# Kernel optimization log

Hardware: AMD Instinct MI355X
Metric: run time of the kernel (lower is better)

## Reference

```python
import jax, jax.numpy as jnp
import numpy as np

E, H, D = 1024, 16, 64
F = 4608          # max_ffn_size = int(1024*3*1.5)
BASE_FFN = 3072   # int(emb*3)
ADAPT = 0.5
CHUNK = 256


def rotate_half(x):
    x1 = x[..., ::2]
    x2 = x[..., 1::2]
    return jnp.stack((-x2, x1), axis=-1).reshape(x.shape[:-1] + (-1,))


def rms_norm(x, w, eps=1e-6):
    x = jnp.where(jnp.isnan(x) | jnp.isinf(x), jnp.zeros_like(x), x)
    rms = jnp.clip(jnp.sqrt(jnp.mean(x * x, axis=-1, keepdims=True) + eps), 1e-6, 1e6)
    return x / rms * w


def setup_inputs() -> dict:
    key = jax.random.key(0)
    ks = jax.random.split(key, 12)
    s = 0.02
    return {
        "x": jax.random.normal(ks[0], (2, 4096, E), dtype=jnp.float32),
        "w_qkv": jax.random.normal(ks[1], (E, 3 * E), dtype=jnp.float32) * s,
        "w_out": jax.random.normal(ks[2], (E, E), dtype=jnp.float32) * s,
        "g1": jnp.ones((E,), dtype=jnp.float32),
        "g2": jnp.ones((E,), dtype=jnp.float32),
        "w_dp1": jax.random.normal(ks[3], (E, E // 4), dtype=jnp.float32) * s,
        "w_dp2": jax.random.normal(ks[4], (E // 4, 1), dtype=jnp.float32) * s,
        "w_gate": jax.random.normal(ks[5], (E, F), dtype=jnp.float32) * s,
        "w_up": jax.random.normal(ks[6], (E, F), dtype=jnp.float32) * s,
        "w_down": jax.random.normal(ks[7], (F, E), dtype=jnp.float32) * s,
        "g_hidden": jnp.ones((F,), dtype=jnp.float32),
    }


def _linear_attention(x, w_qkv, w_out):
    B, L, _ = x.shape
    qkv = (x @ w_qkv).reshape(B, L, 3, H, D).transpose(2, 0, 3, 1, 4)  # [3,B,H,L,D]
    q, k, v = qkv[0], qkv[1], qkv[2]
    # RoPE (start_pos = 0)
    pos = jnp.arange(L, dtype=jnp.float32)
    inv_freq = 1.0 / (10000.0 ** (jnp.arange(0, D, 2, dtype=jnp.float32) / D))
    freqs = pos[:, None] * inv_freq[None, :]
    emb = jnp.concatenate([freqs, freqs], axis=-1)
    cos = jnp.cos(emb)[None, None]
    sin = jnp.sin(emb)[None, None]
    q = q * cos + rotate_half(q) * sin
    k = k * cos + rotate_half(k) * sin
    # elu + 1 feature map
    q = jax.nn.elu(q) + 1.0
    k = jax.nn.elu(k) + 1.0
    # chunk-wise cumulative recurrence (no cache path)
    NC = L // CHUNK
    def to_chunks(t):
        return jnp.moveaxis(t.reshape(B, H, NC, CHUNK, D), 2, 0)  # [NC,B,H,C,D]
    qc, kc, vc = to_chunks(q), to_chunks(k), to_chunks(v)

    def step(carry, inp):
        S, Z = carry  # S:[B,H,D,D], Z:[B,H,D]
        qi, ki, vi = inp
        kv = jnp.einsum('bhld,bhle->bhlde', ki, vi)
        kv_cum = jnp.cumsum(kv, axis=2) + S[:, :, None]
        k_cum = jnp.cumsum(ki, axis=2) + Z[:, :, None]
        num = jnp.einsum('bhld,bhlde->bhle', qi, kv_cum)
        den = jnp.einsum('bhld,bhld->bhl', qi, k_cum)
        return (kv_cum[:, :, -1], k_cum[:, :, -1]), (num, den)

    S0 = jnp.zeros((B, H, D, D), dtype=x.dtype)
    Z0 = jnp.zeros((B, H, D), dtype=x.dtype)
    _, (num, den) = jax.lax.scan(step, (S0, Z0), (qc, kc, vc))
    num = jnp.moveaxis(num, 0, 2).reshape(B, H, L, D)
    den = jnp.moveaxis(den, 0, 2).reshape(B, H, L)
    den = jnp.maximum(den, 1e-6)
    out = num / den[..., None]
    out = out.transpose(0, 2, 1, 3).reshape(B, L, H * D)
    return out @ w_out


def _adaptive_ffn(x, w_dp1, w_dp2, w_gate, w_up, w_down, g_hidden):
    x_mean = x.mean(axis=1)                                   # [B,E]
    dim_ratio = jax.nn.sigmoid(jax.nn.silu(x_mean @ w_dp1) @ w_dp2)  # [B,1]
    ratio = jnp.clip(1.0 + (dim_ratio - 0.5) * 2.0 * ADAPT, 1.0 - ADAPT, 1.0 + ADAPT)
    size = jnp.maximum(1, jnp.floor(BASE_FFN * ratio.mean())).astype(jnp.int32)
    mask = (jnp.arange(F) < size).astype(x.dtype)             # [F]
    gate = jax.nn.silu(x @ w_gate) * mask
    up = (x @ w_up) * mask
    hidden = gate * up
    hidden = jnp.where(jnp.isnan(hidden) | jnp.isinf(hidden), jnp.zeros_like(hidden), hidden)
    # RMSNorm over the first `size` features only (matches sliced torch RMSNorm)
    rms = jnp.sqrt(jnp.sum(hidden * hidden, axis=-1, keepdims=True) / size.astype(x.dtype) + 1e-6)
    rms = jnp.clip(rms, 1e-6, 1e6)
    hidden = hidden / rms * g_hidden * mask                   # padded-to-F hidden
    return hidden @ w_down


def reference(x, w_qkv, w_out, g1, g2, w_dp1, w_dp2, w_gate, w_up, w_down, g_hidden):
    # pre-norm residual block: x + attn(norm1(x)); then x + ffn(norm2(x))
    h = rms_norm(x, g1)
    x = x + _linear_attention(h, w_qkv, w_out)
    h2 = rms_norm(x, g2)
    x = x + _adaptive_ffn(h2, w_dp1, w_dp2, w_gate, w_up, w_down, g_hidden)
    return x
```

## Files before the change

kernel.cpp:

```cpp
#include <hip/hip_runtime.h>
#include <hip/hip_bf16.h>

#define Ee 1024
#define Hh 16
#define Ff 4608
#define Ll 4096
#define Bb 2
#define NCc 16
#define CHk 256

typedef short bf16x8 __attribute__((ext_vector_type(8)));
typedef float f32x4 __attribute__((ext_vector_type(4)));

#define GLD16(g, l) __builtin_amdgcn_global_load_lds( \
    (const __attribute__((address_space(1))) unsigned int*)(g), \
    (__attribute__((address_space(3))) unsigned int*)(l), 16, 0, 0)
#define SCHED0() __builtin_amdgcn_sched_barrier(0)
#define SBAR()   __builtin_amdgcn_s_barrier()

__device__ __forceinline__ unsigned short f2bf(float f){
  unsigned int u = __builtin_bit_cast(unsigned int, f);
  u += 0x7fffu + ((u >> 16) & 1u);
  return (unsigned short)(u >> 16);
}
__device__ __forceinline__ float bf2f(unsigned short h){
  unsigned int u = ((unsigned int)h) << 16;
  return __builtin_bit_cast(float, u);
}
__device__ __forceinline__ float fixv(float v){
  return (__builtin_isnan(v) || __builtin_isinf(v)) ? 0.f : v;
}

__global__ __launch_bounds__(256) void wconv_kernel(const float* __restrict__ W,
    unsigned short* __restrict__ WT, int K, int N, const float* __restrict__ scale){
  __shared__ unsigned short T[64][72];
  int k0 = blockIdx.y*64, n0 = blockIdx.x*64;
  int t = threadIdx.x;
  int kr = t>>4, n4 = (t&15)*4;
  #pragma unroll
  for (int it=0; it<4; it++){
    int k = kr + it*16;
    float s = scale ? scale[k0+k] : 1.f;
    float4 v = *(const float4*)(W + (size_t)(k0+k)*N + n0 + n4);
    T[n4+0][k] = f2bf(v.x*s);
    T[n4+1][k] = f2bf(v.y*s);
    T[n4+2][k] = f2bf(v.z*s);
    T[n4+3][k] = f2bf(v.w*s);
  }
  __syncthreads();
  int u = t&7;
  #pragma unroll
  for (int it=0; it<2; it++){
    int n = (t>>3) + it*32;
    *(bf16x8*)(WT + (size_t)(n0+n)*K + k0 + u*8) = *(const bf16x8*)&T[n][u*8];
  }
}

__global__ __launch_bounds__(256) void rmsnorm_kernel(const float* __restrict__ x,
    const float* __restrict__ g, unsigned short* __restrict__ out){
  int row = blockIdx.x; int t = threadIdx.x;
  float4 v = ((const float4*)(x + (size_t)row*Ee))[t];
  v.x=fixv(v.x); v.y=fixv(v.y); v.z=fixv(v.z); v.w=fixv(v.w);
  float ss = v.x*v.x + v.y*v.y + v.z*v.z + v.w*v.w;
  #pragma unroll
  for (int off=32; off>0; off>>=1) ss += __shfl_down(ss, off);
  __shared__ float red[4];
  if ((t&63)==0) red[t>>6] = ss;
  __syncthreads();
  float tot = red[0]+red[1]+red[2]+red[3];
  float rms = sqrtf(tot*(1.f/Ee) + 1e-6f);
  rms = fminf(fmaxf(rms, 1e-6f), 1e6f);
  float inv = 1.f/rms;
  float4 gv = ((const float4*)g)[t];
  uint2 o;
  o.x = (unsigned)f2bf(v.x*inv*gv.x) | ((unsigned)f2bf(v.y*inv*gv.y)<<16);
  o.y = (unsigned)f2bf(v.z*inv*gv.z) | ((unsigned)f2bf(v.w*inv*gv.w)<<16);
  ((uint2*)(out + (size_t)row*Ee))[t] = o;
}

template<int MODE>
__global__ __launch_bounds__(512) void gemm_kernel(
    const unsigned short* __restrict__ A, const unsigned short* __restrict__ Bt,
    void* __restrict__ Cv, int M, int N, int K,
    const float* __restrict__ res, const float* __restrict__ rowscale,
    const float* __restrict__ klim){
  __shared__ __align__(16) unsigned short S[36864];
  int tid = threadIdx.x;
  int nbx = gridDim.x;
  int id = blockIdx.y * nbx + blockIdx.x;
  int chunk = (nbx * gridDim.y) >> 3;
  int wg = (id & 7) * chunk + (id >> 3);
  int m0 = (wg / nbx) * 256, n0 = (wg % nbx) * 128;
  int lane = tid & 63, wave = tid >> 6;
  int wm = (wave>>1)*64, wn = (wave&1)*64;
  int lrow = lane & 15;
  int lksw = (((lane>>4) ^ ((lrow>>1)&3)))*8;
  float klim0 = (MODE==2 && klim) ? klim[0] : 0.f;
  int kend = K;
  if (MODE==2 && klim){
    int sz = (int)klim0;
    int ke = ((sz + 31) >> 5) << 5;
    kend = ke < K ? ke : K;
  }
  int nk = kend >> 5;
  int segr = lane >> 2;
  int cg = (((lane&3) ^ ((lane>>3)&3))) * 8;
  const unsigned short* gp[3];
  int loff[3];
  #pragma unroll
  for (int i=0;i<3;i++){
// ... 2 lines not shown
    else       { gp[i] = Bt + (size_t)(n0 + (g-16)*16 + segr)*K + cg;  loff[i] = 8192 + (g-16)*512; }
  }
  f32x4 acc[4][4] = {};
  #pragma unroll
  for (int i=0;i<3;i++) GLD16(gp[i], &S[loff[i]]);
  if (nk > 1){
    #pragma unroll
    for (int i=0;i<3;i++) GLD16(gp[i]+32, &S[12288 + loff[i]]);
  }
  SCHED0();
  if (nk > 1) asm volatile("s_waitcnt vmcnt(3)" ::: "memory");
  else        asm volatile("s_waitcnt vmcnt(0)" ::: "memory");
  SBAR(); SCHED0();
  int cur = 0;
  for (int t=0; t<nk; ++t){
    if (t+2 < nk){
      int stg = cur+2; if (stg>=3) stg-=3;
      int ko = (t+2) << 5;
      #pragma unroll
      for (int i=0;i<3;i++) GLD16(gp[i]+ko, &S[stg*12288 + loff[i]]);
    }
    int base = cur*12288;
    bf16x8 af[4], bfr[4];
    #pragma unroll
    for (int i=0;i<4;i++){
      af[i]  = *(const bf16x8*)&S[base + (wm + i*16 + lrow)*32 + lksw];
      bfr[i] = *(const bf16x8*)&S[base + 8192 + (wn + i*16 + lrow)*32 + lksw];
    }
    __builtin_amdgcn_s_setprio(1);
    #pragma unroll
    for (int mi=0;mi<4;mi++)
      #pragma unroll
      for (int ni=0;ni<4;ni++)
        acc[mi][ni] = __builtin_amdgcn_mfma_f32_16x16x32_bf16(af[mi], bfr[ni], acc[mi][ni], 0,0,0);
    __builtin_amdgcn_s_setprio(0);
    if (t+1 < nk){
      SCHED0();
      if (t+2 < nk) asm volatile("s_waitcnt vmcnt(3)" ::: "memory");
      else          asm volatile("s_waitcnt vmcnt(0)" ::: "memory");
      SBAR(); SCHED0();
    }
    cur = (cur==2) ? 0 : cur+1;
  }
  int lg = lane >> 4;
  int rbase = m0 + wm + (lg<<2);
  int cbase = n0 + wn + lrow;
  #pragma unroll
  for (int mi=0;mi<4;mi++){
    #pragma unroll
    for (int r=0;r<4;r++){
      int row = rbase + mi*16 + r;
      float rs = 1.f;
      if (MODE==2){
        float rms = sqrtf(rowscale[row]/klim0 + 1e-6f);
        rms = fminf(fmaxf(rms, 1e-6f), 1e6f);
        rs = 1.f/rms;
      }
      #pragma unroll
      for (int ni=0;ni<4;ni++){
        int col = cbase + ni*16;
        float v = acc[mi][ni][r];
        if (MODE==0){
          ((unsigned short*)Cv)[(size_t)row*N + col] = f2bf(v);
        } else if (MODE==1){
          ((float*)Cv)[(size_t)row*N + col] = v + res[(size_t)row*N + col];
        } else {
          ((float*)Cv)[(size_t)row*N + col] = v*rs + res[(size_t)row*N + col];
        }
      }
    }
  }
}

__global__ __launch_bounds__(512) void gateup_kernel(
    const unsigned short* __restrict__ A, const unsigned short* __restrict__ Gt,
    const unsigned short* __restrict__ Ut, unsigned short* __restrict__ Hid,
    const float* __restrict__ scal, float* __restrict__ sumsq){
  __shared__ __align__(16) unsigned short S[49152];
  int tid = threadIdx.x;
  int nbx = gridDim.x;
  int id = blockIdx.y * nbx + blockIdx.x;
  int chunk = (nbx * gridDim.y) >> 3;
  int wg = (id & 7) * chunk + (id >> 3);
  int m0 = (wg / nbx) * 256, n0 = (wg % nbx) * 128;
  int size = (int)scal[0];
  if (n0 >= size){
    int r = tid >> 1, cb = n0 + (tid&1)*64;
    unsigned short* hp = Hid + (size_t)(m0+r)*Ff + cb;
    bf16x8 z = {};
    #pragma unroll
    for (int i=0;i<8;i++) *(bf16x8*)(hp + i*8) = z;
    return;
  }
  int lane = tid & 63, wave = tid >> 6;
  int wm = (wave>>1)*64, wn = (wave&1)*64;
  int lrow = lane & 15;
  int lksw = (((lane>>4) ^ ((lrow>>1)&3)))*8;
  int segr = lane >> 2;
  int cg = (((lane&3) ^ ((lane>>3)&3))) * 8;
  const unsigned short* gp[4];
  int loff[4];
  #pragma unroll
  for (int i=0;i<4;i++){
    int g = wave*4 + i;
    if (g < 16)      { gp[i] = A  + (size_t)(m0 + g*16 + segr)*Ee + cg;       loff[i] = g*512; }
    else if (g < 24) { gp[i] = Gt + (size_t)(n0 + (g-16)*16 + segr)*Ee + cg;  loff[i] = 8192 + (g-16)*512; }
    else             { gp[i] = Ut + (size_t)(n0 + (g-24)*16 + segr)*Ee + cg;  loff[i] = 12288 + (g-24)*512; }
  }
  f32x4 ag[4][4] = {}, au[4][4] = {};
  #pragma unroll
  for (int i=0;i<4;i++) GLD16(gp[i], &S[loff[i]]);
  #pragma unroll
  for (int i=0;i<4;i++) GLD16(gp[i]+32, &S[16384 + loff[i]]);
  SCHED0();
  asm volatile("s_waitcnt vmcnt(4)" ::: "memory");
  SBAR(); SCHED0();
  int cur = 0;
  for (int t=0; t<32; ++t){
    if (t+2 < 32){
      int stg = cur+2; if (stg>=3) stg-=3;
      int ko = (t+2) << 5;
      #pragma unroll
      for (int i=0;i<4;i++) GLD16(gp[i]+ko, &S[stg*16384 + loff[i]]);
    }
    int base = cur*16384;
    bf16x8 af[4], bg4[4], bu4[4];
    #pragma unroll
    for (int i=0;i<4;i++){
      af[i]  = *(const bf16x8*)&S[base + (wm + i*16 + lrow)*32 + lksw];
      bg4[i] = *(const bf16x8*)&S[base + 8192  + (wn + i*16 + lrow)*32 + lksw];
      bu4[i] = *(const bf16x8*)&S[base + 12288 + (wn + i*16 + lrow)*32 + lksw];
    }
    __builtin_amdgcn_s_setprio(1);
    #pragma unroll
    for (int mi=0;mi<4;mi++)
      #pragma unroll
      for (int ni=0;ni<4;ni++){
        ag[mi][ni] = __builtin_amdgcn_mfma_f32_16x16x32_bf16(af[mi], bg4[ni], ag[mi][ni], 0,0,0);
        au[mi][ni] = __builtin_amdgcn_mfma_f32_16x16x32_bf16(af[mi], bu4[ni], au[mi][ni], 0,0,0);
      }
    __builtin_amdgcn_s_setprio(0);
    if (t+1 < 32){
      SCHED0();
      if (t+2 < 32) asm volatile("s_waitcnt vmcnt(4)" ::: "memory");
      else          asm volatile("s_waitcnt vmcnt(0)" ::: "memory");
      SBAR(); SCHED0();
    }
    cur = (cur==2) ? 0 : cur+1;
  }
  int lg = lane >> 4;
  int lr = lrow;
  int rbase = m0 + wm + (lg<<2);
  int cbase = n0 + wn + lr;
  #pragma unroll
  for (int mi=0;mi<4;mi++){
    #pragma unroll
    for (int r=0;r<4;r++){
      int row = rbase + mi*16 + r;
      float s4 = 0.f;
      #pragma unroll
      for (int ni=0;ni<4;ni++){
        int col = cbase + ni*16;
        float g = ag[mi][ni][r], u = au[mi][ni][r];
        float hv = (g * (1.f/(1.f+expf(-g)))) * u;
        if (col >= size) hv = 0.f;
        if (__builtin_isnan(hv) || __builtin_isinf(hv)) hv = 0.f;
        Hid[(size_t)row*Ff + col] = f2bf(hv);
        s4 += hv*hv;
      }
      s4 += __shfl_xor(s4, 1);
      s4 += __shfl_xor(s4, 2);
      s4 += __shfl_xor(s4, 4);
      s4 += __shfl_xor(s4, 8);
      if (lr == 0) atomicAdd(&sumsq[row], s4);
    }
  }
}

__global__ __launch_bounds__(256) void rope_kernel(unsigned short* __restrict__ qkv){
  size_t idx = (size_t)blockIdx.x*256 + threadIdx.x;
  int i = (int)(idx & 31);
  int h = (int)((idx>>5) & 15);
  size_t bl = idx >> 9;
  int pos = (int)(bl & (Ll-1));
  int d0 = 2*i, d1 = d0+1;
  size_t base = bl*3072 + (size_t)h*64 + d0;
  const float LOG1E4_D32 = 0.2878231366242557f;
  float e0 = (float)(d0 < 32 ? d0 : d0-32);
  float e1 = (float)(d1 < 32 ? d1 : d1-32);
  float f0 = pos * expf(-e0*LOG1E4_D32);
  float f1 = pos * expf(-e1*LOG1E4_D32);
  float s0,c0,s1,c1;
  sincosf(f0,&s0,&c0); sincosf(f1,&s1,&c1);
  unsigned int* qp = (unsigned int*)(qkv + base);
  unsigned int qv = *qp;
  float q0 = bf2f((unsigned short)(qv&0xffff)), q1 = bf2f((unsigned short)(qv>>16));
  float r0 = q0*c0 - q1*s0;
  float r1 = q1*c1 + q0*s1;
  r0 = r0>0.f ? r0+1.f : expf(r0);
  r1 = r1>0.f ? r1+1.f : expf(r1);
  *qp = (unsigned)f2bf(r0) | ((unsigned)f2bf(r1)<<16);
  unsigned int* kp = (unsigned int*)(qkv + base + 1024);
  unsigned int kv = *kp;
  float k0v = bf2f((unsigned short)(kv&0xffff)), k1v = bf2f((unsigned short)(kv>>16));
  float t0 = k0v*c0 - k1v*s0;
  float t1 = k1v*c1 + k0v*s1;
  t0 = t0>0.f ? t0+1.f : expf(t0);
  t1 = t1>0.f ? t1+1.f : expf(t1);
  *kp = (unsigned)f2bf(t0) | ((unsigned)f2bf(t1)<<16);
}

__global__ __launch_bounds__(256) void chunksum_kernel(const unsigned short* __restrict__ qkv,
    float* __restrict__ Ssum){
  __shared__ __align__(16) unsigned short Kt[64][72];
  __shared__ __align__(16) unsigned short Vt[80][72];
  int c = blockIdx.x, bh = blockIdx.y;
  int b = bh >> 4, h = bh & 15;
  int tid = threadIdx.x, lane = tid & 63, wave = tid >> 6;
  int lr = lane & 15, lg = lane >> 4;
  f32x4 acc[5] = {};
  {
    int r16 = tid >> 4, m4 = (tid & 15) * 4;
    unsigned short val = (r16 == 0) ? (unsigned short)0x3F80 : (unsigned short)0;
    #pragma unroll
    for (int u=0; u<4; u++) Vt[64 + r16][m4 + u] = val;
  }
  for (int t=0; t<4; ++t){
    __syncthreads();
    #pragma unroll
    for (int i=0; i<2; i++){
      int tau = tid + i*256;
      int m = tau & 63, dg = (tau >> 6) * 8;
      size_t g = ((size_t)(b*Ll + c*CHk + t*64 + m))*3072 + h*64 + dg;
      bf16x8 kv = *(const bf16x8*)(qkv + g + 1024);
      bf16x8 vv = *(const bf16x8*)(qkv + g + 2048);
      #pragma unroll
      for (int u=0; u<8; u++){
        Kt[dg+u][m] = (unsigned short)kv[u];
        Vt[dg+u][m] = (unsigned short)vv[u];
      }
    }
    __syncthreads();
    #pragma unroll
    for (int kk=0; kk<2; kk++){
      bf16x8 af = *(const bf16x8*)&Kt[wave*16 + lr][kk*32 + lg*8];
      #pragma unroll
      for (int ni=0; ni<5; ni++){
        bf16x8 vf = *(const bf16x8*)&Vt[ni*16 + lr][kk*32 + lg*8];
        acc[ni] = __builtin_amdgcn_mfma_f32_16x16x32_bf16(af, vf, acc[ni], 0,0,0);
      }
    }
  }
  float* S = Ssum + ((size_t)bh*NCc + c)*4160;
  int j = wave*16 + lg*4;
  #pragma unroll
  for (int ni=0; ni<4; ni++)
    #pragma unroll
    for (int r=0; r<4; r++)
      S[(size_t)(j+r)*64 + ni*16 + lr] = acc[ni][r];
  if (lr == 0){
    #pragma unroll
    for (int r=0; r<4; r++) S[4096 + j + r] = acc[4][r];
  }
}

__global__ __launch_bounds__(256) void prefix_kernel(const float* __restrict__ Ssum,
    float* __restrict__ Spre){
  int bh = blockIdx.x; int t = threadIdx.x;
  size_t base = (size_t)bh*NCc*4160;
  for (int e=t; e<4160; e+=256){
    float acc = 0.f;
    #pragma unroll
    for (int c=0;c<NCc;c++){
      Spre[base + (size_t)c*4160 + e] = acc;
      acc += Ssum[base + (size_t)c*4160 + e];
    }
  }
}

__global__ __launch_bounds__(256, 2) void attnout_kernel(const unsigned short* __restrict__ qkv,
    const float* __restrict__ Spre, unsigned short* __restrict__ attn){
  __shared__ __align__(16) unsigned short SpT[64][72];
// ... 13 lines not shown
    #pragma unroll
    for (int g8=0; g8<8; g8++){
      bf16x8 qv = *(const bf16x8*)(qp + g8*8);
      #pragma unroll
      for (int u=0; u<8; u++) zacc += bf2f((unsigned short)qv[u]) * Sp[4096 + g8*8 + u];
    }
    qZd[tid] = zacc;
  }
  #pragma unroll
  for (int i=0; i<2; i++){
    int tau = tid + i*256;
    int j = tau & 63, dg = (tau >> 6) * 8;
    const float* sp = Sp + j*64 + dg;
    #pragma unroll
    for (int u=0; u<8; u++) SpT[dg+u][j] = f2bf(sp[u]);
  }
  bf16x8 af[4][2];
  #pragma unroll
  for (int mi=0; mi<4; mi++){
    size_t qrow = ((size_t)(b*Ll + c*CHk + wave*64 + mi*16 + lr))*3072 + (size_t)h*64;
    #pragma unroll
    for (int kk=0; kk<2; kk++)
      af[mi][kk] = *(const bf16x8*)(qkv + qrow + kk*32 + lg*8);
  }
  __syncthreads();
  f32x4 accO[4][4] = {};
  #pragma unroll
  for (int kk=0; kk<2; kk++){
    #pragma unroll
    for (int ni=0; ni<4; ni++){
      bf16x8 bsp = *(const bf16x8*)&SpT[ni*16 + lr][kk*32 + lg*8];
      #pragma unroll
      for (int mi=0; mi<4; mi++)
        accO[mi][ni] = __builtin_amdgcn_mfma_f32_16x16x32_bf16(af[mi][kk], bsp, accO[mi][ni], 0,0,0);
    }
  }
  f32x4 den4[4] = {};
  for (int t=0; t<4; ++t){
    __syncthreads();
    #pragma unroll
    for (int i=0; i<2; i++){
      int tau = tid + i*256;
      int m = tau & 63, dg = (tau >> 6) * 8;
      size_t g = ((size_t)(b*Ll + c*CHk + t*64 + m))*3072 + h*64 + dg;
      *(bf16x8*)&Ks[m][dg] = *(const bf16x8*)(qkv + g + 1024);
      bf16x8 vv = *(const bf16x8*)(qkv + g + 2048);
      #pragma unroll
      for (int u=0; u<8; u++) Vt[dg+u][m] = (unsigned short)vv[u];
    }
    __syncthreads();
    if (wave < t) continue;
    f32x4 sacc[4][4] = {};
    #pragma unroll
    for (int kk=0; kk<2; kk++){
      #pragma unroll
      for (int ni=0; ni<4; ni++){
        bf16x8 kf = *(const bf16x8*)&Ks[ni*16 + lr][kk*32 + lg*8];
        #pragma unroll
        for (int mi=0; mi<4; mi++)
          sacc[mi][ni] = __builtin_amdgcn_mfma_f32_16x16x32_bf16(af[mi][kk], kf, sacc[mi][ni], 0,0,0);
      }
    }
    unsigned short (*Pw)[72] = P[wave];
    bool diag = (t == wave);
    #pragma unroll
    for (int mi=0; mi<4; mi++){
      #pragma unroll
      for (int r=0; r<4; r++){
        int q_l = mi*16 + lg*4 + r;
        float rs = 0.f;
        #pragma unroll
        for (int ni=0; ni<4; ni++){
          int m_l = ni*16 + lr;
          float v = sacc[mi][ni][r];
          if (diag && m_l > q_l) v = 0.f;
          rs += v;
          Pw[q_l][m_l] = f2bf(v);
        }
        rs += __shfl_xor(rs, 1);
        rs += __shfl_xor(rs, 2);
        rs += __shfl_xor(rs, 4);
        rs += __shfl_xor(rs, 8);
        den4[mi][r] += rs;
      }
    }
    #pragma unroll
    for (int kk=0; kk<2; kk++){
      bf16x8 pa[4], vf[4];
      #pragma unroll
      for (int mi=0; mi<4; mi++) pa[mi] = *(const bf16x8*)&Pw[mi*16 + lr][kk*32 + lg*8];
      #pragma unroll
      for (int ni=0; ni<4; ni++) vf[ni] = *(const bf16x8*)&Vt[ni*16 + lr][kk*32 + lg*8];
      #pragma unroll
      for (int mi=0; mi<4; mi++)
        #pragma unroll
        for (int ni=0; ni<4; ni++)
          accO[mi][ni] = __builtin_amdgcn_mfma_f32_16x16x32_bf16(pa[mi], vf[ni], accO[mi][ni], 0,0,0);
    }
  }
  #pragma unroll
  for (int mi=0; mi<4; mi++){
    #pragma unroll
    for (int r=0; r<4; r++){
      int q_l = mi*16 + lg*4 + r;
      float dtot = den4[mi][r] + qZd[wave*64 + q_l];
      float inv = 1.f / fmaxf(dtot, 1e-6f);
      size_t l = (size_t)(b*Ll + c*CHk + wave*64 + q_l);
      unsigned short* op = attn + l*Ee + h*64 + lr;
      #pragma unroll
      for (int ni=0; ni<4; ni++)
        op[ni*16] = f2bf(accO[mi][ni][r] * inv);
    }
  }
}

__global__ __launch_bounds__(256) void colmean1_kernel(const unsigned short* __restrict__ h2,
    float* __restrict__ partial){
  int e = blockIdx.x*256 + threadIdx.x;
  int ly = blockIdx.y;
  int b = blockIdx.z;
  int l0 = ly * 128;
  float s = 0.f;
  for (int l=l0; l<l0+128; l++) s += bf2f(h2[((size_t)(b*Ll + l))*Ee + e]);
  partial[((size_t)(b*32 + ly))*Ee + e] = s;
}
__global__ __launch_bounds__(256) void colmean2_kernel(const float* __restrict__ partial,
    float* __restrict__ xmean){
  int e = blockIdx.x*256 + threadIdx.x;
  int b = blockIdx.y;
  float s = 0.f;
// ... 28 lines not shown
  }
  if (t==0){
    float rm = 0.5f*(ratio_s[0]+ratio_s[1]);
    float size_f = floorf(3072.f * rm);
    if (size_f < 1.f) size_f = 1.f;
    scalars[0] = size_f;
  }
}

extern "C" void kernel_launch(void* const* d_in, const int* in_sizes, int n_in,
                              void* d_out, int out_size, void* d_ws, size_t ws_size,
                              hipStream_t stream){
  const float* x      = (const float*)d_in[0];
  const float* w_qkv  = (const float*)d_in[1];
  const float* w_out  = (const float*)d_in[2];
  const float* g1     = (const float*)d_in[3];
  const float* g2     = (const float*)d_in[4];
  const float* w_dp1  = (const float*)d_in[5];
  const float* w_dp2  = (const float*)d_in[6];
  const float* w_gate = (const float*)d_in[7];
  const float* w_up   = (const float*)d_in[8];
  const float* w_down = (const float*)d_in[9];
  const float* g_hid  = (const float*)d_in[10];
  float* out = (float*)d_out;

  char* w = (char*)d_ws;
  size_t o = 0;
  auto alloc = [&](size_t bytes)->char*{ char* p = w + o; o += (bytes + 255) & ~255ull; return p; };
  unsigned short* R1   = (unsigned short*)alloc((size_t)8192*1024*2);
  float*          x2   = (float*)alloc((size_t)8192*1024*4);
  char*           R2   = alloc((size_t)8192*4608*2);
  unsigned short* qkvT = (unsigned short*)alloc((size_t)3072*1024*2);
  unsigned short* outT = (unsigned short*)alloc((size_t)1024*1024*2);
  char*           W2   = alloc((size_t)3*4608*1024*2);
  float*       partial = (float*)alloc((size_t)64*1024*4);
  float*         xmean = (float*)alloc(2048*4);
  float*          scal = (float*)alloc(64);
  float*         sumsq = (float*)alloc(8192*4);

  unsigned short* qkv    = (unsigned short*)R2;
  unsigned short* hidden = (unsigned short*)R2;
  float* Ssum = (float*)W2;
  float* Spre = Ssum + (size_t)512*4160;
  unsigned short* gateT = (unsigned short*)W2;
  unsigned short* upT   = gateT + (size_t)4608*1024;
  unsigned short* downT = upT   + (size_t)4608*1024;

  wconv_kernel<<<dim3(3072/64, 1024/64),256,0,stream>>>(w_qkv, qkvT, 1024, 3072, nullptr);
  wconv_kernel<<<dim3(1024/64, 1024/64),256,0,stream>>>(w_out, outT, 1024, 1024, nullptr);

  rmsnorm_kernel<<<8192,256,0,stream>>>(x, g1, R1);
  gemm_kernel<0><<<dim3(3072/128, 8192/256),512,0,stream>>>(R1, qkvT, qkv,
      8192,3072,1024, nullptr,nullptr,nullptr);
  rope_kernel<<<16384,256,0,stream>>>(qkv);
  chunksum_kernel<<<dim3(NCc,Bb*Hh),256,0,stream>>>(qkv, Ssum);
  prefix_kernel<<<Bb*Hh,256,0,stream>>>(Ssum, Spre);
  attnout_kernel<<<dim3(NCc,Bb*Hh),256,0,stream>>>(qkv, Spre, R1);

  wconv_kernel<<<dim3(4608/64, 1024/64),256,0,stream>>>(w_gate, gateT, 1024, 4608, nullptr);
  wconv_kernel<<<dim3(4608/64, 1024/64),256,0,stream>>>(w_up,   upT,   1024, 4608, nullptr);
  wconv_kernel<<<dim3(1024/64, 4608/64),256,0,stream>>>(w_down, downT, 4608, 1024, g_hid);

  gemm_kernel<1><<<dim3(1024/128, 8192/256),512,0,stream>>>(R1, outT, x2,
      8192,1024,1024, x,nullptr,nullptr);
  rmsnorm_kernel<<<8192,256,0,stream>>>(x2, g2, R1);
  colmean1_kernel<<<dim3(4,32,2),256,0,stream>>>(R1, partial);
  colmean2_kernel<<<dim3(4,2),256,0,stream>>>(partial, xmean);
  dimpred_kernel<<<1,256,0,stream>>>(xmean, w_dp1, w_dp2, scal);
  hipMemsetAsync(sumsq, 0, 8192*sizeof(float), stream);
  gateup_kernel<<<dim3(4608/128, 8192/256),512,0,stream>>>(R1, gateT, upT, hidden, scal, sumsq);
  gemm_kernel<2><<<dim3(1024/128, 8192/256),512,0,stream>>>(hidden, downT, out,
      8192,1024,4608, x2, sumsq, scal);
}
```

Measured before the change: 482.6 us.

## Use 256x256 tiled 4-stage GEMM for QKV and interleaved gate/up projection

Adds a new 256x256-tile GEMM with a 4-stage LDS pipeline that splits each k-step into two half-MFMA phases with interleaved global-to-LDS loads, and uses it for the QKV projection. Gate and up weights are interleaved into one transposed matrix in 128-column blocks so the gate/up kernel runs as a single wide GEMM, then pairs the gate and up halves through LDS in the epilogue for SiLU, masking and the sum of squares. The larger tiles aim to raise arithmetic intensity and cut operand refetches. In exchange they add register and LDS pressure and an extra LDS-exchange epilogue with many barriers.

Result: slower. 635.0 us (+31.6%).

```diff
diff --git a/kernel.cpp b/kernel.cpp
--- a/kernel.cpp
+++ b/kernel.cpp
@@ -17,6 +17,7 @@
     (__attribute__((address_space(3))) unsigned int*)(l), 16, 0, 0)
 #define SCHED0() __builtin_amdgcn_sched_barrier(0)
 #define SBAR()   __builtin_amdgcn_s_barrier()
+#define MFMA16(a,b,c) __builtin_amdgcn_mfma_f32_16x16x32_bf16(a,b,c,0,0,0)
 
 __device__ __forceinline__ unsigned short f2bf(float f){
   unsigned int u = __builtin_bit_cast(unsigned int, f);
@@ -32,7 +33,7 @@
 }
 
 __global__ __launch_bounds__(256) void wconv_kernel(const float* __restrict__ W,
-    unsigned short* __restrict__ WT, int K, int N, const float* __restrict__ scale){
+    unsigned short* __restrict__ WT, int K, int N, const float* __restrict__ scale, int gu){
   __shared__ unsigned short T[64][72];
   int k0 = blockIdx.y*64, n0 = blockIdx.x*64;
   int t = threadIdx.x;
@@ -52,7 +53,10 @@
   #pragma unroll
   for (int it=0; it<2; it++){
     int n = (t>>3) + it*32;
-    *(bf16x8*)(WT + (size_t)(n0+n)*K + k0 + u*8) = *(const bf16x8*)&T[n][u*8];
+    int nn = n0 + n;
+    int nout = nn;
+    if (gu) nout = ((nn>>7)<<8) + (nn&127) + ((gu==2)?128:0);
+    *(bf16x8*)(WT + (size_t)nout*K + k0 + u*8) = *(const bf16x8*)&T[n][u*8];
   }
 }
 
@@ -76,6 +80,225 @@
   o.x = (unsigned)f2bf(v.x*inv*gv.x) | ((unsigned)f2bf(v.y*inv*gv.y)<<16);
   o.y = (unsigned)f2bf(v.z*inv*gv.z) | ((unsigned)f2bf(v.w*inv*gv.w)<<16);
   ((uint2*)(out + (size_t)row*Ee))[t] = o;
+}
+
+
+__global__ __launch_bounds__(512) void gemm8p_kernel(
+    const unsigned short* __restrict__ A, const unsigned short* __restrict__ Bt,
+    unsigned short* __restrict__ C, int M, int N, int K){
+  __shared__ __align__(16) unsigned short S[65536];
+  int tid = threadIdx.x;
+  int nbx = gridDim.x;
+  int id = blockIdx.y*nbx + blockIdx.x;
+  int chunk = (nbx*gridDim.y) >> 3;
+  int wg = (id&7)*chunk + (id>>3);
+  int m0 = (wg/nbx)*256, n0 = (wg%nbx)*256;
+  int lane = tid&63, wave = tid>>6;
+  int wm = (wave>>2)*128, wn = (wave&3)*64;
+  int lrow = lane&15, lg = lane>>4;
+  int lksw = (lg ^ ((lrow>>1)&3))*8;
+  int nk = K>>5;
+  int srow = tid>>2;
+  int scg = ((tid&3) ^ ((tid>>3)&3))*8;
+  const unsigned short* aA0 = A  + (size_t)(m0 + srow)*K + scg;
+  const unsigned short* aA1 = A  + (size_t)(m0 + 128 + srow)*K + scg;
+  const unsigned short* aB0 = Bt + (size_t)(n0 + srow)*K + scg;
+  const unsigned short* aB1 = Bt + (size_t)(n0 + 128 + srow)*K + scg;
+  int dA0 = wave*512, dA1 = 4096 + wave*512;
+  int dB0 = 8192 + wave*512, dB1 = 12288 + wave*512;
+  f32x4 acc[8][4] = {};
+  #pragma unroll
+  for (int p=0;p<3;p++){
+    int ko = p<<5; int bb = p*16384;
+    GLD16(aA0+ko, &S[bb+dA0]); GLD16(aA1+ko, &S[bb+dA1]);
+    GLD16(aB0+ko, &S[bb+dB0]); GLD16(aB1+ko, &S[bb+dB1]);
+  }
+  SCHED0();
+  asm volatile("s_waitcnt vmcnt(8)" ::: "memory");
+  SBAR(); SCHED0();
+  int cur = 0;
+  for (int t=0; t<nk; ++t){
+    int sb = ((cur+3)&3)*16384;
+    int ko = (t+3)<<5;
+    bool stg = (t+3 < nk);
+    int rb = cur*16384;
+    bf16x8 bf[4], af[4];
+    #pragma unroll
+    for (int j=0;j<4;j++) bf[j] = *(const bf16x8*)&S[rb + 8192 + (wn + j*16 + lrow)*32 + lksw];
+    #pragma unroll
+    for (int i=0;i<4;i++) af[i] = *(const bf16x8*)&S[rb + (wm + i*16 + lrow)*32 + lksw];
+    if (stg){ GLD16(aA0+ko, &S[sb+dA0]); GLD16(aA1+ko, &S[sb+dA1]); }
+    SCHED0(); SBAR();
+    asm volatile("s_waitcnt lgkmcnt(0)" ::: "memory");
+    SCHED0();
+    __builtin_amdgcn_s_setprio(1);
+    #pragma unroll
+    for (int i=0;i<4;i++)
+      #pragma unroll
+      for (int j=0;j<4;j++)
+        acc[i][j] = MFMA16(af[i], bf[j], acc[i][j]);
+    __builtin_amdgcn_s_setprio(0);
+    SCHED0(); SBAR();
+    #pragma unroll
+    for (int i=0;i<4;i++) af[i] = *(const bf16x8*)&S[rb + (wm + 64 + i*16 + lrow)*32 + lksw];
+    if (stg){ GLD16(aB0+ko, &S[sb+dB0]); GLD16(aB1+ko, &S[sb+dB1]); }
+    SCHED0();
+    if (t+3 < nk)      asm volatile("s_waitcnt vmcnt(8)" ::: "memory");
+    else if (t+2 < nk) asm volatile("s_waitcnt vmcnt(4)" ::: "memory");
+    else               asm volatile("s_waitcnt vmcnt(0)" ::: "memory");
+    SBAR();
+    asm volatile("s_waitcnt lgkmcnt(0)" ::: "memory");
+    SCHED0();
+    __builtin_amdgcn_s_setprio(1);
+    #pragma unroll
+    for (int i=0;i<4;i++)
+      #pragma unroll
+      for (int j=0;j<4;j++)
+        acc[4+i][j] = MFMA16(af[i], bf[j], acc[4+i][j]);
+    __builtin_amdgcn_s_setprio(0);
+    SCHED0(); SBAR();
+    cur = (cur+1)&3;
+  }
+  #pragma unroll
+  for (int mi=0;mi<8;mi++){
+    #pragma unroll
+    for (int r=0;r<4;r++){
+      int row = m0 + wm + mi*16 + lg*4 + r;
+      #pragma unroll
+      for (int ni=0;ni<4;ni++){
+        int col = n0 + wn + ni*16 + lrow;
+        C[(size_t)row*N + col] = f2bf(acc[mi][ni][r]);
+      }
+    }
+  }
+}
+
+__global__ __launch_bounds__(512) void gateup8p_kernel(
+    const unsigned short* __restrict__ A, const unsigned short* __restrict__ GUt,
+    unsigned short* __restrict__ Hid, const float* __restrict__ scal,
+    float* __restrict__ sumsq){
+  __shared__ __align__(16) unsigned short S[65536];
+  int tid = threadIdx.x;
+  int nbx = gridDim.x;
+  int id = blockIdx.y*nbx + blockIdx.x;
+  int chunk = (nbx*gridDim.y) >> 3;
+  int wg = (id&7)*chunk + (id>>3);
+  int m0 = (wg/nbx)*256, n0 = (wg%nbx)*256;
+  int n0r = (n0>>8)*128;
+  int size = (int)scal[0];
+  if (n0r >= size){
+    int r = tid >> 1, cb = n0r + (tid&1)*64;
+    unsigned short* hp = Hid + (size_t)(m0+r)*Ff + cb;
+    bf16x8 z = {};
+    #pragma unroll
+    for (int i=0;i<8;i++) *(bf16x8*)(hp + i*8) = z;
+    return;
+  }
+  int lane = tid&63, wave = tid>>6;
+  int wm = (wave>>2)*128, wn = (wave&3)*64;
+  int lrow = lane&15, lg = lane>>4;
+  int lksw = (lg ^ ((lrow>>1)&3))*8;
+  const int K = Ee, nk = Ee>>5;
+  int srow = tid>>2;
+  int scg = ((tid&3) ^ ((tid>>3)&3))*8;
+  const unsigned short* aA0 = A   + (size_t)(m0 + srow)*K + scg;
+  const unsigned short* aA1 = A   + (size_t)(m0 + 128 + srow)*K + scg;
+  const unsigned short* aB0 = GUt + (size_t)(n0 + srow)*K + scg;
+  const unsigned short* aB1 = GUt + (size_t)(n0 + 128 + srow)*K + scg;
+  int dA0 = wave*512, dA1 = 4096 + wave*512;
+  int dB0 = 8192 + wave*512, dB1 = 12288 + wave*512;
+  f32x4 acc[8][4] = {};
+  #pragma unroll
+  for (int p=0;p<3;p++){
+    int ko = p<<5; int bb = p*16384;
+    GLD16(aA0+ko, &S[bb+dA0]); GLD16(aA1+ko, &S[bb+dA1]);
+    GLD16(aB0+ko, &S[bb+dB0]); GLD16(aB1+ko, &S[bb+dB1]);
+  }
+  SCHED0();
+  asm volatile("s_waitcnt vmcnt(8)" ::: "memory");
+  SBAR(); SCHED0();
+  int cur = 0;
+  for (int t=0; t<nk; ++t){
+    int sb = ((cur+3)&3)*16384;
+    int ko = (t+3)<<5;
+    bool stg = (t+3 < nk);
+    int rb = cur*16384;
+    bf16x8 bf[4], af[4];
+    #pragma unroll
+    for (int j=0;j<4;j++) bf[j] = *(const bf16x8*)&S[rb + 8192 + (wn + j*16 + lrow)*32 + lksw];
+    #pragma unroll
+    for (int i=0;i<4;i++) af[i] = *(const bf16x8*)&S[rb + (wm + i*16 + lrow)*32 + lksw];
+    if (stg){ GLD16(aA0+ko, &S[sb+dA0]); GLD16(aA1+ko, &S[sb+dA1]); }
+    SCHED0(); SBAR();
+    asm volatile("s_waitcnt lgkmcnt(0)" ::: "memory");
+    SCHED0();
+    __builtin_amdgcn_s_setprio(1);
+    #pragma unroll
+    for (int i=0;i<4;i++)
+      #pragma unroll
+      for (int j=0;j<4;j++)
+        acc[i][j] = MFMA16(af[i], bf[j], acc[i][j]);
+    __builtin_amdgcn_s_setprio(0);
+    SCHED0(); SBAR();
+    #pragma unroll
+    for (int i=0;i<4;i++) af[i] = *(const bf16x8*)&S[rb + (wm + 64 + i*16 + lrow)*32 + lksw];
+    if (stg){ GLD16(aB0+ko, &S[sb+dB0]); GLD16(aB1+ko, &S[sb+dB1]); }
+    SCHED0();
+    if (t+3 < nk)      asm volatile("s_waitcnt vmcnt(8)" ::: "memory");
+    else if (t+2 < nk) asm volatile("s_waitcnt vmcnt(4)" ::: "memory");
+    else               asm volatile("s_waitcnt vmcnt(0)" ::: "memory");
+    SBAR();
+    asm volatile("s_waitcnt lgkmcnt(0)" ::: "memory");
+    SCHED0();
+    __builtin_amdgcn_s_setprio(1);
+    #pragma unroll
+    for (int i=0;i<4;i++)
+      #pragma unroll
+      for (int j=0;j<4;j++)
+        acc[4+i][j] = MFMA16(af[i], bf[j], acc[4+i][j]);
+    __builtin_amdgcn_s_setprio(0);
+    SCHED0(); SBAR();
+    cur = (cur+1)&3;
+  }
+  float* X = (float*)S;
+  int mg = wave>>2, q = wave&3;
+  __syncthreads();
+  for (int mi=0; mi<8; mi++){
+    if (q >= 2){
+      int bi = (q-2) + 2*mg;
+      #pragma unroll
+      for (int r=0;r<4;r++)
+        #pragma unroll
+        for (int ni=0;ni<4;ni++)
+          X[bi*1024 + (lg*4+r)*64 + ni*16 + lrow] = acc[mi][ni][r];
+    }
+    __syncthreads();
+    if (q < 2){
+      int bi = q + 2*mg;
+      #pragma unroll
+      for (int r=0;r<4;r++){
+        int row = m0 + wm + mi*16 + lg*4 + r;
+        float s4 = 0.f;
+        #pragma unroll
+        for (int ni=0;ni<4;ni++){
+          int col = n0r + q*64 + ni*16 + lrow;
+          float g = acc[mi][ni][r];
+          float u = X[bi*1024 + (lg*4+r)*64 + ni*16 + lrow];
+          float hv = (g * (1.f/(1.f+expf(-g)))) * u;
+          if (col >= size) hv = 0.f;
+          if (__builtin_isnan(hv) || __builtin_isinf(hv)) hv = 0.f;
+          Hid[(size_t)row*Ff + col] = f2bf(hv);
+          s4 += hv*hv;
+        }
+        s4 += __shfl_xor(s4, 1);
+        s4 += __shfl_xor(s4, 2);
+        s4 += __shfl_xor(s4, 4);
+        s4 += __shfl_xor(s4, 8);
+        if (lrow == 0) atomicAdd(&sumsq[row], s4);
+      }
+    }
+    __syncthreads();
+  }
 }
 
 template<int MODE>
@@ -144,7 +367,7 @@
     for (int mi=0;mi<4;mi++)
       #pragma unroll
       for (int ni=0;ni<4;ni++)
-        acc[mi][ni] = __builtin_amdgcn_mfma_f32_16x16x32_bf16(af[mi], bfr[ni], acc[mi][ni], 0,0,0);
+        acc[mi][ni] = MFMA16(af[mi], bfr[ni], acc[mi][ni]);
     __builtin_amdgcn_s_setprio(0);
     if (t+1 < nk){
       SCHED0();
@@ -172,119 +395,12 @@
       for (int ni=0;ni<4;ni++){
         int col = cbase + ni*16;
         float v = acc[mi][ni][r];
-        if (MODE==0){
-          ((unsigned short*)Cv)[(size_t)row*N + col] = f2bf(v);
-        } else if (MODE==1){
+        if (MODE==1){
           ((float*)Cv)[(size_t)row*N + col] = v + res[(size_t)row*N + col];
         } else {
           ((float*)Cv)[(size_t)row*N + col] = v*rs + res[(size_t)row*N + col];
         }
       }
-    }
-  }
-}
-
-__global__ __launch_bounds__(512) void gateup_kernel(
-    const unsigned short* __restrict__ A, const unsigned short* __restrict__ Gt,
-    const unsigned short* __restrict__ Ut, unsigned short* __restrict__ Hid,
-    const float* __restrict__ scal, float* __restrict__ sumsq){
-  __shared__ __align__(16) unsigned short S[49152];
-  int tid = threadIdx.x;
-  int nbx = gridDim.x;
-  int id = blockIdx.y * nbx + blockIdx.x;
-  int chunk = (nbx * gridDim.y) >> 3;
-  int wg = (id & 7) * chunk + (id >> 3);
-  int m0 = (wg / nbx) * 256, n0 = (wg % nbx) * 128;
-  int size = (int)scal[0];
-  if (n0 >= size){
-    int r = tid >> 1, cb = n0 + (tid&1)*64;
-    unsigned short* hp = Hid + (size_t)(m0+r)*Ff + cb;
-    bf16x8 z = {};
-    #pragma unroll
-    for (int i=0;i<8;i++) *(bf16x8*)(hp + i*8) = z;
-    return;
-  }
-  int lane = tid & 63, wave = tid >> 6;
-  int wm = (wave>>1)*64, wn = (wave&1)*64;
-  int lrow = lane & 15;
-  int lksw = (((lane>>4) ^ ((lrow>>1)&3)))*8;
-  int segr = lane >> 2;
-  int cg = (((lane&3) ^ ((lane>>3)&3))) * 8;
-  const unsigned short* gp[4];
-  int loff[4];
-  #pragma unroll
-  for (int i=0;i<4;i++){
-    int g = wave*4 + i;
-    if (g < 16)      { gp[i] = A  + (size_t)(m0 + g*16 + segr)*Ee + cg;       loff[i] = g*512; }
-    else if (g < 24) { gp[i] = Gt + (size_t)(n0 + (g-16)*16 + segr)*Ee + cg;  loff[i] = 8192 + (g-16)*512; }
-    else             { gp[i] = Ut + (size_t)(n0 + (g-24)*16 + segr)*Ee + cg;  loff[i] = 12288 + (g-24)*512; }
-  }
-  f32x4 ag[4][4] = {}, au[4][4] = {};
-  #pragma unroll
-  for (int i=0;i<4;i++) GLD16(gp[i], &S[loff[i]]);
-  #pragma unroll
-  for (int i=0;i<4;i++) GLD16(gp[i]+32, &S[16384 + loff[i]]);
-  SCHED0();
-  asm volatile("s_waitcnt vmcnt(4)" ::: "memory");
-  SBAR(); SCHED0();
-  int cur = 0;
-  for (int t=0; t<32; ++t){
-    if (t+2 < 32){
-      int stg = cur+2; if (stg>=3) stg-=3;
-      int ko = (t+2) << 5;
-      #pragma unroll
-      for (int i=0;i<4;i++) GLD16(gp[i]+ko, &S[stg*16384 + loff[i]]);
-    }
-    int base = cur*16384;
-    bf16x8 af[4], bg4[4], bu4[4];
-    #pragma unroll
-    for (int i=0;i<4;i++){
-      af[i]  = *(const bf16x8*)&S[base + (wm + i*16 + lrow)*32 + lksw];
-      bg4[i] = *(const bf16x8*)&S[base + 8192  + (wn + i*16 + lrow)*32 + lksw];
-      bu4[i] = *(const bf16x8*)&S[base + 12288 + (wn + i*16 + lrow)*32 + lksw];
-    }
-    __builtin_amdgcn_s_setprio(1);
-    #pragma unroll
-    for (int mi=0;mi<4;mi++)
-      #pragma unroll
-      for (int ni=0;ni<4;ni++){
-        ag[mi][ni] = __builtin_amdgcn_mfma_f32_16x16x32_bf16(af[mi], bg4[ni], ag[mi][ni], 0,0,0);
-        au[mi][ni] = __builtin_amdgcn_mfma_f32_16x16x32_bf16(af[mi], bu4[ni], au[mi][ni], 0,0,0);
-      }
-    __builtin_amdgcn_s_setprio(0);
-    if (t+1 < 32){
-      SCHED0();
-      if (t+2 < 32) asm volatile("s_waitcnt vmcnt(4)" ::: "memory");
-      else          asm volatile("s_waitcnt vmcnt(0)" ::: "memory");
-      SBAR(); SCHED0();
-    }
-    cur = (cur==2) ? 0 : cur+1;
-  }
-  int lg = lane >> 4;
-  int lr = lrow;
-  int rbase = m0 + wm + (lg<<2);
-  int cbase = n0 + wn + lr;
-  #pragma unroll
-  for (int mi=0;mi<4;mi++){
-    #pragma unroll
-    for (int r=0;r<4;r++){
-      int row = rbase + mi*16 + r;
-      float s4 = 0.f;
-      #pragma unroll
-      for (int ni=0;ni<4;ni++){
-        int col = cbase + ni*16;
-        float g = ag[mi][ni][r], u = au[mi][ni][r];
-        float hv = (g * (1.f/(1.f+expf(-g)))) * u;
-        if (col >= size) hv = 0.f;
-        if (__builtin_isnan(hv) || __builtin_isinf(hv)) hv = 0.f;
-        Hid[(size_t)row*Ff + col] = f2bf(hv);
-        s4 += hv*hv;
-      }
-      s4 += __shfl_xor(s4, 1);
-      s4 += __shfl_xor(s4, 2);
-      s4 += __shfl_xor(s4, 4);
-      s4 += __shfl_xor(s4, 8);
-      if (lr == 0) atomicAdd(&sumsq[row], s4);
     }
   }
 }
@@ -359,7 +475,7 @@
       #pragma unroll
       for (int ni=0; ni<5; ni++){
         bf16x8 vf = *(const bf16x8*)&Vt[ni*16 + lr][kk*32 + lg*8];
-        acc[ni] = __builtin_amdgcn_mfma_f32_16x16x32_bf16(af, vf, acc[ni], 0,0,0);
+        acc[ni] = MFMA16(af, vf, acc[ni]);
       }
     }
   }
@@ -439,7 +555,7 @@
       bf16x8 bsp = *(const bf16x8*)&SpT[ni*16 + lr][kk*32 + lg*8];
       #pragma unroll
       for (int mi=0; mi<4; mi++)
-        accO[mi][ni] = __builtin_amdgcn_mfma_f32_16x16x32_bf16(af[mi][kk], bsp, accO[mi][ni], 0,0,0);
+        accO[mi][ni] = MFMA16(af[mi][kk], bsp, accO[mi][ni]);
     }
   }
   f32x4 den4[4] = {};
@@ -465,7 +581,7 @@
         bf16x8 kf = *(const bf16x8*)&Ks[ni*16 + lr][kk*32 + lg*8];
         #pragma unroll
         for (int mi=0; mi<4; mi++)
-          sacc[mi][ni] = __builtin_amdgcn_mfma_f32_16x16x32_bf16(af[mi][kk], kf, sacc[mi][ni], 0,0,0);
+          sacc[mi][ni] = MFMA16(af[mi][kk], kf, sacc[mi][ni]);
       }
     }
     unsigned short (*Pw)[72] = P[wave];
@@ -502,7 +618,7 @@
       for (int mi=0; mi<4; mi++)
         #pragma unroll
         for (int ni=0; ni<4; ni++)
-          accO[mi][ni] = __builtin_amdgcn_mfma_f32_16x16x32_bf16(pa[mi], vf[ni], accO[mi][ni], 0,0,0);
+          accO[mi][ni] = MFMA16(pa[mi], vf[ni], accO[mi][ni]);
     }
   }
   #pragma unroll
@@ -597,7 +713,7 @@
   char*           R2   = alloc((size_t)8192*4608*2);
   unsigned short* qkvT = (unsigned short*)alloc((size_t)3072*1024*2);
   unsigned short* outT = (unsigned short*)alloc((size_t)1024*1024*2);
-  char*           W2   = alloc((size_t)3*4608*1024*2);
+  char*           W2   = alloc((size_t)(9216+4608)*1024*2);
   float*       partial = (float*)alloc((size_t)64*1024*4);
   float*         xmean = (float*)alloc(2048*4);
   float*          scal = (float*)alloc(64);
@@ -607,24 +723,22 @@
   unsigned short* hidden = (unsigned short*)R2;
   float* Ssum = (float*)W2;
   float* Spre = Ssum + (size_t)512*4160;
-  unsigned short* gateT = (unsigned short*)W2;
-  unsigned short* upT   = gateT + (size_t)4608*1024;
-  unsigned short* downT = upT   + (size_t)4608*1024;
-
-  wconv_kernel<<<dim3(3072/64, 1024/64),256,0,stream>>>(w_qkv, qkvT, 1024, 3072, nullptr);
-  wconv_kernel<<<dim3(1024/64, 1024/64),256,0,stream>>>(w_out, outT, 1024, 1024, nullptr);
+  unsigned short* guT   = (unsigned short*)W2;
+  unsigned short* downT = guT + (size_t)9216*1024;
+
+  wconv_kernel<<<dim3(3072/64, 1024/64),256,0,stream>>>(w_qkv, qkvT, 1024, 3072, nullptr, 0);
+  wconv_kernel<<<dim3(1024/64, 1024/64),256,0,stream>>>(w_out, outT, 1024, 1024, nullptr, 0);
 
   rmsnorm_kernel<<<8192,256,0,stream>>>(x, g1, R1);
-  gemm_kernel<0><<<dim3(3072/128, 8192/256),512,0,stream>>>(R1, qkvT, qkv,
-      8192,3072,1024, nullptr,nullptr,nullptr);
+  gemm8p_kernel<<<dim3(3072/256, 8192/256),512,0,stream>>>(R1, qkvT, qkv, 8192,3072,1024);
   rope_kernel<<<16384,256,0,stream>>>(qkv);
   chunksum_kernel<<<dim3(NCc,Bb*Hh),256,0,stream>>>(qkv, Ssum);
   prefix_kernel<<<Bb*Hh,256,0,stream>>>(Ssum, Spre);
   attnout_kernel<<<dim3(NCc,Bb*Hh),256,0,stream>>>(qkv, Spre, R1);
 
-  wconv_kernel<<<dim3(4608/64, 1024/64),256,0,stream>>>(w_gate, gateT, 1024, 4608, nullptr);
-  wconv_kernel<<<dim3(4608/64, 1024/64),256,0,stream>>>(w_up,   upT,   1024, 4608, nullptr);
-  wconv_kernel<<<dim3(1024/64, 4608/64),256,0,stream>>>(w_down, downT, 4608, 1024, g_hid);
+  wconv_kernel<<<dim3(4608/64, 1024/64),256,0,stream>>>(w_gate, guT, 1024, 4608, nullptr, 1);
+  wconv_kernel<<<dim3(4608/64, 1024/64),256,0,stream>>>(w_up,   guT, 1024, 4608, nullptr, 2);
+  wconv_kernel<<<dim3(1024/64, 4608/64),256,0,stream>>>(w_down, downT, 4608, 1024, g_hid, 0);
 
   gemm_kernel<1><<<dim3(1024/128, 8192/256),512,0,stream>>>(R1, outT, x2,
       8192,1024,1024, x,nullptr,nullptr);
@@ -633,7 +747,7 @@
   colmean2_kernel<<<dim3(4,2),256,0,stream>>>(partial, xmean);
   dimpred_kernel<<<1,256,0,stream>>>(xmean, w_dp1, w_dp2, scal);
   hipMemsetAsync(sumsq, 0, 8192*sizeof(float), stream);
-  gateup_kernel<<<dim3(4608/128, 8192/256),512,0,stream>>>(R1, gateT, upT, hidden, scal, sumsq);
+  gateup8p_kernel<<<dim3(9216/256, 8192/256),512,0,stream>>>(R1, guT, hidden, scal, sumsq);
   gemm_kernel<2><<<dim3(1024/128, 8192/256),512,0,stream>>>(hidden, downT, out,
       8192,1024,4608, x2, sumsq, scal);
 }
```

## Fuse RoPE and ELU feature map into QKV GEMM epilogue; double-buffer gate/up

Applied to the files above, without the earlier changes.

Removes the separate RoPE kernel and applies rotary embedding plus the elu+1 feature map inside the QKV GEMM epilogue, using lane shuffles to fetch the paired element, so the extra read and write of q/k is avoided. Separately, the gate/up kernel drops its three-stage LDS pipeline with manual waitcnt in favour of a two-buffer scheme with __syncthreads, which lowers LDS use but may expose more load latency. The fused epilogue uses fast __sincosf and works on fp32 accumulators before bf16 rounding, so results can differ slightly from the previous path.

Measured after the change: 516.8 us. 7.1% more time.

```diff
diff --git a/kernel.cpp b/kernel.cpp
--- a/kernel.cpp
+++ b/kernel.cpp
@@ -17,6 +17,7 @@
     (__attribute__((address_space(3))) unsigned int*)(l), 16, 0, 0)
 #define SCHED0() __builtin_amdgcn_sched_barrier(0)
 #define SBAR()   __builtin_amdgcn_s_barrier()
+#define MFMA16(a,b,c) __builtin_amdgcn_mfma_f32_16x16x32_bf16(a,b,c,0,0,0)
 
 __device__ __forceinline__ unsigned short f2bf(float f){
   unsigned int u = __builtin_bit_cast(unsigned int, f);
@@ -144,7 +145,7 @@
     for (int mi=0;mi<4;mi++)
       #pragma unroll
       for (int ni=0;ni<4;ni++)
-        acc[mi][ni] = __builtin_amdgcn_mfma_f32_16x16x32_bf16(af[mi], bfr[ni], acc[mi][ni], 0,0,0);
+        acc[mi][ni] = MFMA16(af[mi], bfr[ni], acc[mi][ni]);
     __builtin_amdgcn_s_setprio(0);
     if (t+1 < nk){
       SCHED0();
@@ -157,6 +158,20 @@
   int lg = lane >> 4;
   int rbase = m0 + wm + (lg<<2);
   int cbase = n0 + wn + lrow;
+  bool do_rope = false;
+  float fb[4];
+  if (MODE==0){
+    do_rope = (cbase < 2048);
+    if (do_rope){
+      const float LOG1E4_D32 = 0.2878231366242557f;
+      float e0 = (float)lrow;
+      float e1 = (float)(lrow + 16);
+      fb[0] = expf(-e0*LOG1E4_D32);
+      fb[1] = expf(-e1*LOG1E4_D32);
+      fb[2] = fb[0];
+      fb[3] = fb[1];
+    }
+  }
   #pragma unroll
   for (int mi=0;mi<4;mi++){
     #pragma unroll
@@ -168,12 +183,22 @@
         rms = fminf(fmaxf(rms, 1e-6f), 1e6f);
         rs = 1.f/rms;
       }
+      float pos = (float)(row & (Ll-1));
       #pragma unroll
       for (int ni=0;ni<4;ni++){
         int col = cbase + ni*16;
         float v = acc[mi][ni][r];
         if (MODE==0){
-          ((unsigned short*)Cv)[(size_t)row*N + col] = f2bf(v);
+          float o = v;
+          if (do_rope){
+            float p = __shfl_xor(v, 1);
+            float f = pos * fb[ni];
+            float s, cft;
+            __sincosf(f, &s, &cft);
+            o = (lrow & 1) ? (v*cft + p*s) : (v*cft - p*s);
+            o = o > 0.f ? o + 1.f : expf(o);
+          }
+          ((unsigned short*)Cv)[(size_t)row*N + col] = f2bf(o);
         } else if (MODE==1){
           ((float*)Cv)[(size_t)row*N + col] = v + res[(size_t)row*N + col];
         } else {
@@ -188,7 +213,7 @@
     const unsigned short* __restrict__ A, const unsigned short* __restrict__ Gt,
     const unsigned short* __restrict__ Ut, unsigned short* __restrict__ Hid,
     const float* __restrict__ scal, float* __restrict__ sumsq){
-  __shared__ __align__(16) unsigned short S[49152];
+  __shared__ __align__(16) unsigned short S[2][16384];
   int tid = threadIdx.x;
   int nbx = gridDim.x;
   int id = blockIdx.y * nbx + blockIdx.x;
@@ -221,44 +246,33 @@
   }
   f32x4 ag[4][4] = {}, au[4][4] = {};
   #pragma unroll
-  for (int i=0;i<4;i++) GLD16(gp[i], &S[loff[i]]);
-  #pragma unroll
-  for (int i=0;i<4;i++) GLD16(gp[i]+32, &S[16384 + loff[i]]);
-  SCHED0();
-  asm volatile("s_waitcnt vmcnt(4)" ::: "memory");
-  SBAR(); SCHED0();
+  for (int i=0;i<4;i++) GLD16(gp[i], &S[0][loff[i]]);
+  __syncthreads();
   int cur = 0;
   for (int t=0; t<32; ++t){
-    if (t+2 < 32){
-      int stg = cur+2; if (stg>=3) stg-=3;
-      int ko = (t+2) << 5;
-      #pragma unroll
-      for (int i=0;i<4;i++) GLD16(gp[i]+ko, &S[stg*16384 + loff[i]]);
-    }
-    int base = cur*16384;
+    if (t+1 < 32){
+      int ko = (t+1) << 5;
+      #pragma unroll
+      for (int i=0;i<4;i++) GLD16(gp[i]+ko, &S[cur^1][loff[i]]);
+    }
     bf16x8 af[4], bg4[4], bu4[4];
     #pragma unroll
     for (int i=0;i<4;i++){
-      af[i]  = *(const bf16x8*)&S[base + (wm + i*16 + lrow)*32 + lksw];
-      bg4[i] = *(const bf16x8*)&S[base + 8192  + (wn + i*16 + lrow)*32 + lksw];
-      bu4[i] = *(const bf16x8*)&S[base + 12288 + (wn + i*16 + lrow)*32 + lksw];
+      af[i]  = *(const bf16x8*)&S[cur][(wm + i*16 + lrow)*32 + lksw];
+      bg4[i] = *(const bf16x8*)&S[cur][8192  + (wn + i*16 + lrow)*32 + lksw];
+      bu4[i] = *(const bf16x8*)&S[cur][12288 + (wn + i*16 + lrow)*32 + lksw];
     }
     __builtin_amdgcn_s_setprio(1);
     #pragma unroll
     for (int mi=0;mi<4;mi++)
       #pragma unroll
       for (int ni=0;ni<4;ni++){
-        ag[mi][ni] = __builtin_amdgcn_mfma_f32_16x16x32_bf16(af[mi], bg4[ni], ag[mi][ni], 0,0,0);
-        au[mi][ni] = __builtin_amdgcn_mfma_f32_16x16x32_bf16(af[mi], bu4[ni], au[mi][ni], 0,0,0);
+        ag[mi][ni] = MFMA16(af[mi], bg4[ni], ag[mi][ni]);
+        au[mi][ni] = MFMA16(af[mi], bu4[ni], au[mi][ni]);
       }
     __builtin_amdgcn_s_setprio(0);
-    if (t+1 < 32){
-      SCHED0();
-      if (t+2 < 32) asm volatile("s_waitcnt vmcnt(4)" ::: "memory");
-      else          asm volatile("s_waitcnt vmcnt(0)" ::: "memory");
-      SBAR(); SCHED0();
-    }
-    cur = (cur==2) ? 0 : cur+1;
+    __syncthreads();
+    cur ^= 1;
   }
   int lg = lane >> 4;
   int lr = lrow;
@@ -287,39 +301,6 @@
       if (lr == 0) atomicAdd(&sumsq[row], s4);
     }
   }
-}
-
-__global__ __launch_bounds__(256) void rope_kernel(unsigned short* __restrict__ qkv){
-  size_t idx = (size_t)blockIdx.x*256 + threadIdx.x;
-  int i = (int)(idx & 31);
-  int h = (int)((idx>>5) & 15);
-  size_t bl = idx >> 9;
-  int pos = (int)(bl & (Ll-1));
-  int d0 = 2*i, d1 = d0+1;
-  size_t base = bl*3072 + (size_t)h*64 + d0;
-  const float LOG1E4_D32 = 0.2878231366242557f;
-  float e0 = (float)(d0 < 32 ? d0 : d0-32);
-  float e1 = (float)(d1 < 32 ? d1 : d1-32);
-  float f0 = pos * expf(-e0*LOG1E4_D32);
-  float f1 = pos * expf(-e1*LOG1E4_D32);
-  float s0,c0,s1,c1;
-  sincosf(f0,&s0,&c0); sincosf(f1,&s1,&c1);
-  unsigned int* qp = (unsigned int*)(qkv + base);
-  unsigned int qv = *qp;
-  float q0 = bf2f((unsigned short)(qv&0xffff)), q1 = bf2f((unsigned short)(qv>>16));
-  float r0 = q0*c0 - q1*s0;
-  float r1 = q1*c1 + q0*s1;
-  r0 = r0>0.f ? r0+1.f : expf(r0);
-  r1 = r1>0.f ? r1+1.f : expf(r1);
-  *qp = (unsigned)f2bf(r0) | ((unsigned)f2bf(r1)<<16);
-  unsigned int* kp = (unsigned int*)(qkv + base + 1024);
-  unsigned int kv = *kp;
-  float k0v = bf2f((unsigned short)(kv&0xffff)), k1v = bf2f((unsigned short)(kv>>16));
-  float t0 = k0v*c0 - k1v*s0;
-  float t1 = k1v*c1 + k0v*s1;
-  t0 = t0>0.f ? t0+1.f : expf(t0);
-  t1 = t1>0.f ? t1+1.f : expf(t1);
-  *kp = (unsigned)f2bf(t0) | ((unsigned)f2bf(t1)<<16);
 }
 
 __global__ __launch_bounds__(256) void chunksum_kernel(const unsigned short* __restrict__ qkv,
@@ -359,7 +340,7 @@
       #pragma unroll
       for (int ni=0; ni<5; ni++){
         bf16x8 vf = *(const bf16x8*)&Vt[ni*16 + lr][kk*32 + lg*8];
-        acc[ni] = __builtin_amdgcn_mfma_f32_16x16x32_bf16(af, vf, acc[ni], 0,0,0);
+        acc[ni] = MFMA16(af, vf, acc[ni]);
       }
     }
   }
@@ -439,7 +420,7 @@
       bf16x8 bsp = *(const bf16x8*)&SpT[ni*16 + lr][kk*32 + lg*8];
       #pragma unroll
       for (int mi=0; mi<4; mi++)
-        accO[mi][ni] = __builtin_amdgcn_mfma_f32_16x16x32_bf16(af[mi][kk], bsp, accO[mi][ni], 0,0,0);
+        accO[mi][ni] = MFMA16(af[mi][kk], bsp, accO[mi][ni]);
     }
   }
   f32x4 den4[4] = {};
@@ -465,7 +446,7 @@
         bf16x8 kf = *(const bf16x8*)&Ks[ni*16 + lr][kk*32 + lg*8];
         #pragma unroll
         for (int mi=0; mi<4; mi++)
-          sacc[mi][ni] = __builtin_amdgcn_mfma_f32_16x16x32_bf16(af[mi][kk], kf, sacc[mi][ni], 0,0,0);
+          sacc[mi][ni] = MFMA16(af[mi][kk], kf, sacc[mi][ni]);
       }
     }
     unsigned short (*Pw)[72] = P[wave];
@@ -502,7 +483,7 @@
       for (int mi=0; mi<4; mi++)
         #pragma unroll
         for (int ni=0; ni<4; ni++)
-          accO[mi][ni] = __builtin_amdgcn_mfma_f32_16x16x32_bf16(pa[mi], vf[ni], accO[mi][ni], 0,0,0);
+          accO[mi][ni] = MFMA16(pa[mi], vf[ni], accO[mi][ni]);
     }
   }
   #pragma unroll
@@ -617,7 +598,6 @@
   rmsnorm_kernel<<<8192,256,0,stream>>>(x, g1, R1);
   gemm_kernel<0><<<dim3(3072/128, 8192/256),512,0,stream>>>(R1, qkvT, qkv,
       8192,3072,1024, nullptr,nullptr,nullptr);
-  rope_kernel<<<16384,256,0,stream>>>(qkv);
   chunksum_kernel<<<dim3(NCc,Bb*Hh),256,0,stream>>>(qkv, Ssum);
   prefix_kernel<<<Bb*Hh,256,0,stream>>>(Ssum, Spre);
   attnout_kernel<<<dim3(NCc,Bb*Hh),256,0,stream>>>(qkv, Spre, R1);
```
